# Performance work log

Hardware: AMD Instinct MI355X
Metric: run time of the kernel (lower is better)

The kernel has to match this reference:

```python
import jax, jax.numpy as jnp
import numpy as np

BATCH, SEQ, F_DIM, R_DIM, OUT_DIM = 128, 1024, 256, 64, 1024


def setup_inputs() -> dict:
    key = jax.random.key(0)
    k1, k2, k3, k4, k5 = jax.random.split(key, 5)
    fillers = jax.random.normal(k1, (BATCH, SEQ, F_DIM), dtype=jnp.float32)
    roles = jax.random.normal(k2, (BATCH, SEQ, R_DIM), dtype=jnp.float32)
    lengths = jax.random.randint(k3, (BATCH,), 0, SEQ, dtype=jnp.int64)
    # nn.Linear(filler_dim*role_dim, output_dim): weight (out, in), bias (out,)
    bound = 1.0 / np.sqrt(F_DIM * R_DIM)
    W = jax.random.uniform(k4, (OUT_DIM, F_DIM * R_DIM), minval=-bound, maxval=bound, dtype=jnp.float32)
    b = jax.random.uniform(k5, (OUT_DIM,), minval=-bound, maxval=bound, dtype=jnp.float32)
    return {"fillers": fillers, "roles": roles, "lengths": lengths, "W": W, "b": b}


def reference(fillers, roles, lengths, W, b):
    batch, seq_len, f_dim = fillers.shape
    r_dim = roles.shape[-1]
    # mask[b, s] = s < lengths[b]
    mask = (jnp.arange(seq_len)[None, :] < lengths[:, None]).astype(fillers.dtype)
    # Fuse mask into fillers, then contract over seq directly:
    # sum_s mask * (fillers[b,s,:] outer roles[b,s,:]) == (mask*fillers)^T @ roles per batch
    # Avoids materializing the (b, s, e, r) intermediate; same math as the torch module.
    tensor_sum = jnp.einsum('bse,bsr->ber', fillers * mask[:, :, None], roles)  # (b, e, r)
    tensor_flat = tensor_sum.reshape(batch, f_dim * r_dim)
    return tensor_flat @ W.T + b
```

## Files before the change

kernel.cpp:

```cpp
#include <hip/hip_runtime.h>
#include <hip/hip_bf16.h>

#define NB 128
#define NS 1024
#define NE 256
#define NR 64
#define NO 1024
#define NK (NE*NR)

typedef __attribute__((ext_vector_type(8))) short short8;
typedef __attribute__((ext_vector_type(4))) float float4v;
typedef __attribute__((ext_vector_type(4))) unsigned short ushort4v;
typedef __attribute__((ext_vector_type(8))) unsigned short ushort8v;
typedef __attribute__((ext_vector_type(4))) unsigned int uint4v;

static __device__ inline unsigned short f2bf(float x) {
    union { float f; unsigned u; } v; v.f = x;
    unsigned r = v.u + 0x7fffu + ((v.u >> 16) & 1u);
    return (unsigned short)(r >> 16);
}
static __device__ inline float bf2f(unsigned short h) {
    union { unsigned u; float f; } v; v.u = ((unsigned)h) << 16;
    return v.f;
}
static __device__ inline unsigned pk(float lo, float hi) {
    union { __hip_bfloat162 h2; unsigned u; } v;
    v.h2.x = __float2bfloat16(lo);
    v.h2.y = __float2bfloat16(hi);
    return v.u;
}

#define NCH 8
#define PSTEP 16
#define SA 260
#define SB 68

__global__ __launch_bounds__(512, 4) void k1_mfma(
    const float* __restrict__ fillers, const float* __restrict__ roles,
    const int* __restrict__ lengths, unsigned short* __restrict__ parts)
{
    __shared__ unsigned As32[PSTEP * SA];
    __shared__ unsigned Bs32[PSTEP * SB];

    const int bid = blockIdx.x;
    const int b   = bid & 127;
    const int ch  = (bid >> 7) & 7;
    const int len = lengths[b];
    const int tid = threadIdx.x;

    const int lane = tid & 63;
    const int wid  = tid >> 6;
    const int lrow = lane & 15;
    const int lgrp = lane >> 4;
    const int we   = wid >> 1;
    const int wn   = wid & 1;
    const int qb   = tid >> 4;
    const int r4   = tid & 15;

    const int P      = (len + 1) >> 1;
    const int count  = (P > ch) ? ((P - ch + 7) >> 3) : 0;
    const int nsteps = (count + PSTEP - 1) >> 4;

    const float4 zf4 = make_float4(0.f, 0.f, 0.f, 0.f);
    const float* fb = fillers + (size_t)b * NS * NE;
    const float* rb = roles   + (size_t)b * NS * NR;
    unsigned short* pp = parts + (size_t)(ch * NB + b) * NK;

    float4v acc[4][2];
    #pragma unroll
    for (int i = 0; i < 4; ++i)
        #pragma unroll
        for (int j = 0; j < 2; ++j)
            acc[i][j] = (float4v){0.f, 0.f, 0.f, 0.f};

    float4 Ast[2][2];
    float4 Bst[2];

    #define K1_STAGE(t)                                                     \
    {                                                                       \
        const int base = (t) * PSTEP;                                       \
        const int smax = 2 * (ch + 8 * (base + 15)) + 1;                    \
        const bool edge = (smax >= len);                 \
        _Pragma("unroll")                                                   \
        for (int i = 0; i < 2; ++i) {                                       \
            const int c = tid + 512 * i;                                    \
            const int q = c >> 6, e4 = c & 63;                              \
            const int s0 = 2 * (ch + 8 * (base + q));                       \
            const float* f0 = fb + (size_t)s0 * NE + e4 * 4;                \
            float4 v0 = *(const float4*)f0;                                 \
            float4 v1 = *(const float4*)(f0 + NE);                          \
            if (edge) {                                                     \
                if (s0     >= len) v0 = zf4;                                \
                if (s0 + 1 >= len) v1 = zf4;                                \
            }                                                               \
            Ast[i][0] = v0; Ast[i][1] = v1;                                 \
        }                                                                   \
        if (tid < 256) {                                                    \
            const int s0 = 2 * (ch + 8 * (base + qb));                      \
            const float* r0 = rb + (size_t)s0 * NR + r4 * 4;                \
            float4 v0 = *(const float4*)r0;                                 \
            float4 v1 = *(const float4*)(r0 + NR);                          \
            if (edge) {                                                     \
                if (s0     >= len) v0 = zf4;                                \
                if (s0 + 1 >= len) v1 = zf4;                                \
            }                                                               \
            Bst[0] = v0; Bst[1] = v1;                                       \
        }                                                                   \
    }

    if (nsteps > 0) K1_STAGE(0);

    for (int t = 0; t < nsteps; ++t) {
        __syncthreads();

        #pragma unroll
        for (int i = 0; i < 2; ++i) {
            const int c = tid + 512 * i;
            const int q = c >> 6, e4 = c & 63;
            uint4v w;
            w.x = pk(Ast[i][0].x, Ast[i][1].x);
            w.y = pk(Ast[i][0].y, Ast[i][1].y);
            w.z = pk(Ast[i][0].z, Ast[i][1].z);
            w.w = pk(Ast[i][0].w, Ast[i][1].w);
            *(uint4v*)&As32[q * SA + e4 * 4] = w;
        }
        if (tid < 256) {
            uint4v w;
            w.x = pk(Bst[0].x, Bst[1].x);
            w.y = pk(Bst[0].y, Bst[1].y);
            w.z = pk(Bst[0].z, Bst[1].z);
            w.w = pk(Bst[0].w, Bst[1].w);
            *(uint4v*)&Bs32[qb * SB + r4 * 4] = w;
        }

        __syncthreads();

        if (t + 1 < nsteps) K1_STAGE(t + 1);

        union { unsigned u[4]; short8 s8; } af[4], bf[2];
        #pragma unroll
        for (int mf = 0; mf < 4; ++mf) {
            const int e = we * 64 + mf * 16 + lrow;
            #pragma unroll
            for (int jj = 0; jj < 4; ++jj)
                af[mf].u[jj] = As32[(lgrp * 4 + jj) * SA + e];
        }
        #pragma unroll
        for (int nf = 0; nf < 2; ++nf) {
            const int r = wn * 32 + nf * 16 + lrow;
            #pragma unroll
            for (int jj = 0; jj < 4; ++jj)
                bf[nf].u[jj] = Bs32[(lgrp * 4 + jj) * SB + r];
        }
        #pragma unroll
        for (int mf = 0; mf < 4; ++mf)
            #pragma unroll
            for (int nf = 0; nf < 2; ++nf)
                acc[mf][nf] = __builtin_amdgcn_mfma_f32_16x16x32_bf16(
                    af[mf].s8, bf[nf].s8, acc[mf][nf], 0, 0, 0);
    }

    #pragma unroll
    for (int mf = 0; mf < 4; ++mf) {
        #pragma unroll
        for (int nf = 0; nf < 2; ++nf) {
            const int r = wn * 32 + nf * 16 + lrow;
            #pragma unroll
            for (int reg = 0; reg < 4; ++reg) {
                const int e = we * 64 + mf * 16 + lgrp * 4 + reg;
                pp[(size_t)e * NR + r] = f2bf(acc[mf][nf][reg]);
            }
        }
    }
    #undef K1_STAGE
}

__global__ __launch_bounds__(256) void k1b_reduce(
    const unsigned short* __restrict__ parts, unsigned short* __restrict__ tensor)
{
    const size_t i = ((size_t)blockIdx.x * 256 + threadIdx.x) * 8;
    float s[8] = {0.f,0.f,0.f,0.f,0.f,0.f,0.f,0.f};
    #pragma unroll
    for (int ch = 0; ch < NCH; ++ch) {
        ushort8v v = *(const ushort8v*)(parts + (size_t)ch * NB * NK + i);
        #pragma unroll
        for (int j = 0; j < 8; ++j)
            s[j] += bf2f(v[j]);
    }
    ushort8v o;
    #pragma unroll
    for (int j = 0; j < 8; ++j)
        o[j] = f2bf(s[j]);
    *(ushort8v*)(tensor + i) = o;
}

#define BN2 64
#define BK2 128
#define KSPLIT 32
#define KC2 (NK/KSPLIT)

__global__ __launch_bounds__(512) void k2_mfma(
    const unsigned short* __restrict__ A,
    const float* __restrict__ W,
    float* __restrict__ part)
{
    __shared__ unsigned short As[128 * BK2];
    __shared__ unsigned short Bs[BN2 * BK2];

    const int o0   = blockIdx.x * BN2;
    const int kz   = blockIdx.y;
    const int tid  = threadIdx.x;
    const int lane = tid & 63;
    const int wid  = tid >> 6;
    const int wm   = wid >> 1;
    const int wn   = wid & 1;
    const int lrow = lane & 15;
    const int lgrp = lane >> 4;

    float4v acc[2][2];
    #pragma unroll
    for (int i = 0; i < 2; ++i)
        #pragma unroll
        for (int j = 0; j < 2; ++j)
            acc[i][j] = (float4v){0.f, 0.f, 0.f, 0.f};

    ushort8v av[4];
    float4   wv[4];

    #define K2_LOAD(step)                                                   \
    {                                                                       \
        const int kb = kz * KC2 + (step) * BK2;                             \
        _Pragma("unroll")                                                   \
        for (int i = 0; i < 4; ++i) {                                       \
            const int c = tid + 512 * i;                                    \
            const int r = c >> 4, c16 = c & 15;                             \
            av[i] = *(const ushort8v*)(A + (size_t)r * NK + kb + c16 * 8);  \
        }                                                                   \
        _Pragma("unroll")                                                   \
        for (int i = 0; i < 2; ++i) {                                       \
            const int c = tid + 512 * i;                                    \
            const int r = c >> 4, c8 = c & 15;                              \
            const float* wp = W + (size_t)(o0 + r) * NK + kb + c8 * 8;      \
            wv[2*i]   = *(const float4*)wp;                                 \
            wv[2*i+1] = *(const float4*)(wp + 4);                           \
        }                                                                   \
    }

    K2_LOAD(0);

    for (int step = 0; step < KC2 / BK2; ++step) {
        __syncthreads();

        #pragma unroll
        for (int i = 0; i < 4; ++i) {
            const int c = tid + 512 * i;
            const int r = c >> 4, c16 = c & 15;
            const int byte = (r * 256 + c16 * 16) ^ ((r & 7) << 4);
            *(ushort8v*)((char*)As + byte) = av[i];
        }
        #pragma unroll
        for (int i = 0; i < 2; ++i) {
            const int c = tid + 512 * i;
            const int r = c >> 4, c8 = c & 15;
            ushort8v bv;
            bv[0] = f2bf(wv[2*i].x);   bv[1] = f2bf(wv[2*i].y);
            bv[2] = f2bf(wv[2*i].z);   bv[3] = f2bf(wv[2*i].w);
            bv[4] = f2bf(wv[2*i+1].x); bv[5] = f2bf(wv[2*i+1].y);
            bv[6] = f2bf(wv[2*i+1].z); bv[7] = f2bf(wv[2*i+1].w);
            const int byte = (r * 256 + c8 * 16) ^ ((r & 7) << 4);
            *(ushort8v*)((char*)Bs + byte) = bv;
        }

        __syncthreads();

        if (step + 1 < KC2 / BK2) K2_LOAD(step + 1);

        #pragma unroll
        for (int kk = 0; kk < BK2; kk += 32) {
            short8 af[2], bf[2];
            #pragma unroll
            for (int mf = 0; mf < 2; ++mf) {
                const int r = wm * 32 + mf * 16 + lrow;
                const int byte = (r * 256 + (kk + lgrp * 8) * 2) ^ ((r & 7) << 4);
                af[mf] = *(const short8*)((const char*)As + byte);
            }
            #pragma unroll
            for (int nf = 0; nf < 2; ++nf) {
                const int r = wn * 32 + nf * 16 + lrow;
                const int byte = (r * 256 + (kk + lgrp * 8) * 2) ^ ((r & 7) << 4);
                bf[nf] = *(const short8*)((const char*)Bs + byte);
            }
            #pragma unroll
            for (int mf = 0; mf < 2; ++mf)
                #pragma unroll
                for (int nf = 0; nf < 2; ++nf)
                    acc[mf][nf] = __builtin_amdgcn_mfma_f32_16x16x32_bf16(
                        af[mf], bf[nf], acc[mf][nf], 0, 0, 0);
        }
    }

    float* pbase = part + (size_t)kz * NB * NO;
    #pragma unroll
    for (int mf = 0; mf < 2; ++mf) {
        #pragma unroll
        for (int nf = 0; nf < 2; ++nf) {
            const int o = o0 + wn * 32 + nf * 16 + lrow;
            #pragma unroll
            for (int reg = 0; reg < 4; ++reg) {
                const int m = wm * 32 + mf * 16 + lgrp * 4 + reg;
                pbase[(size_t)m * NO + o] = acc[mf][nf][reg];
            }
        }
    }
    #undef K2_LOAD
}

__global__ __launch_bounds__(256) void k3_reduce(
    const float* __restrict__ part, const float* __restrict__ bias,
    float* __restrict__ out)
{
    const int i = (blockIdx.x * 256 + threadIdx.x) * 4;
    float4 v = *(const float4*)(bias + (i & (NO - 1)));
    #pragma unroll
    for (int z = 0; z < KSPLIT; ++z) {
        float4 p = *(const float4*)(part + (size_t)z * NB * NO + i);
        v.x += p.x; v.y += p.y; v.z += p.z; v.w += p.w;
    }
    *(float4*)(out + i) = v;
}

extern "C" void kernel_launch(void* const* d_in, const int* in_sizes, int n_in,
                              void* d_out, int out_size, void* d_ws, size_t ws_size,
                              hipStream_t stream)
{
    const float* fillers = (const float*)d_in[0];
    const float* roles   = (const float*)d_in[1];
    const int*   lengths = (const int*)d_in[2];
    const float* W       = (const float*)d_in[3];
    const float* bias    = (const float*)d_in[4];
    float* out = (float*)d_out;

    unsigned short* tensor = (unsigned short*)d_ws;
    unsigned short* parts  = tensor + (size_t)NB * NK;
    float*          part   = (float*)parts;

    k1_mfma<<<NB * NCH, 512, 0, stream>>>(fillers, roles, lengths, parts);
    k1b_reduce<<<(NB * NK / 8) / 256, 256, 0, stream>>>(parts, tensor);
    dim3 g2(NO / BN2, KSPLIT);
    k2_mfma<<<g2, 512, 0, stream>>>(tensor, W, part);
    k3_reduce<<<(NB * NO) / 1024, 256, 0, stream>>>(part, bias, out);
}
```

Before: 63.33 us.

## Split filler dimension across two blocks and fully unroll the staged k1 pipeline

The first kernel now splits the 256-wide filler dimension into two halves, each handled by its own block, which doubles the grid and halves the per-block tile, accumulators and LDS row stride. The sequence loop is replaced by an explicit schedule of at most four steps using two register buffers, so global loads run two stages ahead of the MFMA work. The aim is more blocks in flight and better latency hiding for the bandwidth-bound filler read. The cost is that each roles tile is now loaded by two blocks. The schedule also relies on nsteps never exceeding four, which holds for these sizes.

```diff
diff --git a/kernel.cpp b/kernel.cpp
--- a/kernel.cpp
+++ b/kernel.cpp
@@ -31,8 +31,9 @@
 }
 
 #define NCH 8
+
 #define PSTEP 16
-#define SA 260
+#define SA 132
 #define SB 68
 
 __global__ __launch_bounds__(512, 4) void k1_mfma(
@@ -44,7 +45,8 @@
 
     const int bid = blockIdx.x;
     const int b   = bid & 127;
-    const int ch  = (bid >> 7) & 7;
+    const int eh  = (bid >> 7) & 1;
+    const int ch  = bid >> 8;
     const int len = lengths[b];
     const int tid = threadIdx.x;
 
@@ -54,6 +56,8 @@
     const int lgrp = lane >> 4;
     const int we   = wid >> 1;
     const int wn   = wid & 1;
+    const int qa   = tid >> 5;
+    const int e4a  = tid & 31;
     const int qb   = tid >> 4;
     const int r4   = tid & 15;
 
@@ -62,38 +66,35 @@
     const int nsteps = (count + PSTEP - 1) >> 4;
 
     const float4 zf4 = make_float4(0.f, 0.f, 0.f, 0.f);
-    const float* fb = fillers + (size_t)b * NS * NE;
+    const float* fb = fillers + (size_t)b * NS * NE + eh * 128;
     const float* rb = roles   + (size_t)b * NS * NR;
-    unsigned short* pp = parts + (size_t)(ch * NB + b) * NK;
-
-    float4v acc[4][2];
-    #pragma unroll
-    for (int i = 0; i < 4; ++i)
+    unsigned short* pp = parts + (size_t)(ch * NB + b) * NK + (size_t)eh * 128 * NR;
+
+    float4v acc[2][2];
+    #pragma unroll
+    for (int i = 0; i < 2; ++i)
         #pragma unroll
         for (int j = 0; j < 2; ++j)
             acc[i][j] = (float4v){0.f, 0.f, 0.f, 0.f};
 
-    float4 Ast[2][2];
-    float4 Bst[2];
-
-    #define K1_STAGE(t)                                                     \
+    float4 A0a, A0b, B0a, B0b;
+    float4 A1a, A1b, B1a, B1b;
+
+    #define K1_STAGE(t, Aa, Ab, Ba, Bb)                                     \
     {                                                                       \
         const int base = (t) * PSTEP;                                       \
         const int smax = 2 * (ch + 8 * (base + 15)) + 1;                    \
         const bool edge = (smax >= len);                 \
-        _Pragma("unroll")                                                   \
-        for (int i = 0; i < 2; ++i) {                                       \
-            const int c = tid + 512 * i;                                    \
-            const int q = c >> 6, e4 = c & 63;                              \
-            const int s0 = 2 * (ch + 8 * (base + q));                       \
-            const float* f0 = fb + (size_t)s0 * NE + e4 * 4;                \
+        {                                                                   \
+            const int s0 = 2 * (ch + 8 * (base + qa));                      \
+            const float* f0 = fb + (size_t)s0 * NE + e4a * 4;               \
             float4 v0 = *(const float4*)f0;                                 \
             float4 v1 = *(const float4*)(f0 + NE);                          \
             if (edge) {                                                     \
                 if (s0     >= len) v0 = zf4;                                \
                 if (s0 + 1 >= len) v1 = zf4;                                \
             }                                                               \
-            Ast[i][0] = v0; Ast[i][1] = v1;                                 \
+            Aa = v0; Ab = v1;                                               \
         }                                                                   \
         if (tid < 256) {                                                    \
             const int s0 = 2 * (ch + 8 * (base + qb));                      \
@@ -104,75 +105,96 @@
                 if (s0     >= len) v0 = zf4;                                \
                 if (s0 + 1 >= len) v1 = zf4;                                \
             }                                                               \
-            Bst[0] = v0; Bst[1] = v1;                                       \
-        }                                                                   \
-    }
-
-    if (nsteps > 0) K1_STAGE(0);
-
-    for (int t = 0; t < nsteps; ++t) {
+            Ba = v0; Bb = v1;                                               \
+        }                                                                   \
+    }
+
+    #define K1_WRITE(Aa, Ab, Ba, Bb)                                        \
+    {                                                                       \
+        {                                                                   \
+            uint4v w;                                                       \
+            w.x = pk(Aa.x, Ab.x);  w.y = pk(Aa.y, Ab.y);                    \
+            w.z = pk(Aa.z, Ab.z);  w.w = pk(Aa.w, Ab.w);                    \
+            *(uint4v*)&As32[qa * SA + e4a * 4] = w;                         \
+        }                                                                   \
+        if (tid < 256) {                                                    \
+            uint4v w;                                                       \
+            w.x = pk(Ba.x, Bb.x);  w.y = pk(Ba.y, Bb.y);                    \
+            w.z = pk(Ba.z, Bb.z);  w.w = pk(Ba.w, Bb.w);                    \
+            *(uint4v*)&Bs32[qb * SB + r4 * 4] = w;                          \
+        }                                                                   \
+    }
+
+    #define K1_MFMA()                                                       \
+    {                                                                       \
+        union { unsigned u[4]; short8 s8; } af[2], bf[2];                   \
+        _Pragma("unroll")                                                   \
+        for (int mf = 0; mf < 2; ++mf) {                                    \
+            const int e = we * 32 + mf * 16 + lrow;                         \
+            _Pragma("unroll")                                               \
+            for (int jj = 0; jj < 4; ++jj)                                  \
+                af[mf].u[jj] = As32[(lgrp * 4 + jj) * SA + e];              \
+        }                                                                   \
+        _Pragma("unroll")                                                   \
+        for (int nf = 0; nf < 2; ++nf) {                                    \
+            const int r = wn * 32 + nf * 16 + lrow;                         \
+            _Pragma("unroll")                                               \
+            for (int jj = 0; jj < 4; ++jj)                                  \
+                bf[nf].u[jj] = Bs32[(lgrp * 4 + jj) * SB + r];              \
+        }                                                                   \
+        _Pragma("unroll")                                                   \
+        for (int mf = 0; mf < 2; ++mf)                                      \
+            _Pragma("unroll")                                               \
+            for (int nf = 0; nf < 2; ++nf)                                  \
+                acc[mf][nf] = __builtin_amdgcn_mfma_f32_16x16x32_bf16(      \
+                    af[mf].s8, bf[nf].s8, acc[mf][nf], 0, 0, 0);            \
+    }
+
+    if (nsteps > 0) {
+        K1_STAGE(0, A0a, A0b, B0a, B0b);
+        if (nsteps > 1) K1_STAGE(1, A1a, A1b, B1a, B1b);
+
+        K1_WRITE(A0a, A0b, B0a, B0b);
         __syncthreads();
-
-        #pragma unroll
-        for (int i = 0; i < 2; ++i) {
-            const int c = tid + 512 * i;
-            const int q = c >> 6, e4 = c & 63;
-            uint4v w;
-            w.x = pk(Ast[i][0].x, Ast[i][1].x);
-            w.y = pk(Ast[i][0].y, Ast[i][1].y);
-            w.z = pk(Ast[i][0].z, Ast[i][1].z);
-            w.w = pk(Ast[i][0].w, Ast[i][1].w);
-            *(uint4v*)&As32[q * SA + e4 * 4] = w;
-        }
-        if (tid < 256) {
-            uint4v w;
-            w.x = pk(Bst[0].x, Bst[1].x);
-            w.y = pk(Bst[0].y, Bst[1].y);
-            w.z = pk(Bst[0].z, Bst[1].z);
-            w.w = pk(Bst[0].w, Bst[1].w);
-            *(uint4v*)&Bs32[qb * SB + r4 * 4] = w;
-        }
-
-        __syncthreads();
-
-        if (t + 1 < nsteps) K1_STAGE(t + 1);
-
-        union { unsigned u[4]; short8 s8; } af[4], bf[2];
-        #pragma unroll
-        for (int mf = 0; mf < 4; ++mf) {
-            const int e = we * 64 + mf * 16 + lrow;
-            #pragma unroll
-            for (int jj = 0; jj < 4; ++jj)
-                af[mf].u[jj] = As32[(lgrp * 4 + jj) * SA + e];
-        }
+        if (nsteps > 2) K1_STAGE(2, A0a, A0b, B0a, B0b);
+        K1_MFMA();
+
+        if (nsteps > 1) {
+            __syncthreads();
+            K1_WRITE(A1a, A1b, B1a, B1b);
+            __syncthreads();
+            if (nsteps > 3) K1_STAGE(3, A1a, A1b, B1a, B1b);
+            K1_MFMA();
+        }
+        if (nsteps > 2) {
+            __syncthreads();
+            K1_WRITE(A0a, A0b, B0a, B0b);
+            __syncthreads();
+            K1_MFMA();
+        }
+        if (nsteps > 3) {
+            __syncthreads();
+            K1_WRITE(A1a, A1b, B1a, B1b);
+            __syncthreads();
+            K1_MFMA();
+        }
+    }
+
+    #pragma unroll
+    for (int mf = 0; mf < 2; ++mf) {
         #pragma unroll
         for (int nf = 0; nf < 2; ++nf) {
             const int r = wn * 32 + nf * 16 + lrow;
             #pragma unroll
-            for (int jj = 0; jj < 4; ++jj)
-                bf[nf].u[jj] = Bs32[(lgrp * 4 + jj) * SB + r];
-        }
-        #pragma unroll
-        for (int mf = 0; mf < 4; ++mf)
-            #pragma unroll
-            for (int nf = 0; nf < 2; ++nf)
-                acc[mf][nf] = __builtin_amdgcn_mfma_f32_16x16x32_bf16(
-                    af[mf].s8, bf[nf].s8, acc[mf][nf], 0, 0, 0);
-    }
-
-    #pragma unroll
-    for (int mf = 0; mf < 4; ++mf) {
-        #pragma unroll
-        for (int nf = 0; nf < 2; ++nf) {
-            const int r = wn * 32 + nf * 16 + lrow;
-            #pragma unroll
             for (int reg = 0; reg < 4; ++reg) {
-                const int e = we * 64 + mf * 16 + lgrp * 4 + reg;
+                const int e = we * 32 + mf * 16 + lgrp * 4 + reg;
                 pp[(size_t)e * NR + r] = f2bf(acc[mf][nf][reg]);
             }
         }
     }
     #undef K1_STAGE
+    #undef K1_WRITE
+    #undef K1_MFMA
 }
 
 __global__ __launch_bounds__(256) void k1b_reduce(
@@ -344,7 +366,7 @@
     unsigned short* parts  = tensor + (size_t)NB * NK;
     float*          part   = (float*)parts;
 
-    k1_mfma<<<NB * NCH, 512, 0, stream>>>(fillers, roles, lengths, parts);
+    k1_mfma<<<NB * NCH * 2, 512, 0, stream>>>(fillers, roles, lengths, parts);
     k1b_reduce<<<(NB * NK / 8) / 256, 256, 0, stream>>>(parts, tensor);
     dim3 g2(NO / BN2, KSPLIT);
     k2_mfma<<<g2, 512, 0, stream>>>(tensor, W, part);
```

Result: no change. 62.90 us (-0.7%).
